# Kernel tuning notes

Hardware: AMD Instinct MI355X
Metric: run time of the kernel (lower is better)

## Reference

```python
import jax, jax.numpy as jnp
import numpy as np

B = 8192
DIMS = [1024, 1024, 1024, 1024]  # input, hidden0, hidden1, output
RANK = 64


def _apg_layer(x, Wm, bm, U, V, b, activate):
    # hyper-net (MLP_Layer with no hidden units == single Linear): generates rank*rank weights per sample
    w = (x @ Wm.T + bm).reshape(x.shape[0], RANK, RANK)   # [B, r, r]
    u = x @ U.T                                           # U_matrix: [B, r]
    # (u.unsqueeze(-1) * w).sum(-2) == per-sample matvec
    h = jnp.einsum('br,brs->bs', u, w)                    # [B, r]
    out = h @ V.T + b                                     # V_matrix + static bias: [B, out]
    return jax.nn.relu(out) if activate else out


def setup_inputs() -> dict:
    key = jax.random.key(0)
    ks = jax.random.split(key, 16)
    inp = {"x": jax.random.normal(ks[0], (B, DIMS[0]), dtype=jnp.float32)}
    ki = 1
    for l in range(3):
        din, dout = DIMS[l], DIMS[l + 1]
        inp[f"Wm{l}"] = jax.random.normal(ks[ki], (RANK * RANK, din), dtype=jnp.float32) * (1.0 / np.sqrt(din)); ki += 1
        inp[f"bm{l}"] = jnp.zeros((RANK * RANK,), dtype=jnp.float32)
        inp[f"U{l}"] = jax.random.normal(ks[ki], (RANK, din), dtype=jnp.float32) * (1.0 / np.sqrt(din)); ki += 1
        inp[f"V{l}"] = jax.random.normal(ks[ki], (dout, RANK), dtype=jnp.float32) * (1.0 / np.sqrt(RANK)); ki += 1
        inp[f"b{l}"] = jnp.zeros((dout,), dtype=jnp.float32)
    return inp


def reference(x, Wm0, bm0, U0, V0, b0, Wm1, bm1, U1, V1, b1, Wm2, bm2, U2, V2, b2):
    h = _apg_layer(x, Wm0, bm0, U0, V0, b0, activate=True)   # hidden layer 0 + ReLU
    h = _apg_layer(h, Wm1, bm1, U1, V1, b1, activate=True)   # hidden layer 1 + ReLU
    out = _apg_layer(h, Wm2, bm2, U2, V2, b2, activate=False)  # output layer, no activation
    return out
```

## Files before the change

kernel.cpp:

```cpp
#include <hip/hip_runtime.h>
#include <stdint.h>

typedef short bf16x8_t __attribute__((ext_vector_type(8)));
typedef short bf16x4_t __attribute__((ext_vector_type(4)));
typedef float f32x4_t __attribute__((ext_vector_type(4)));
typedef unsigned short u16x4_t __attribute__((ext_vector_type(4)));
typedef unsigned short u16x8_t __attribute__((ext_vector_type(8)));

#define DEV static __device__ __forceinline__

DEV float bf2f(unsigned short u) {
  union { unsigned int i; float f; } v; v.i = ((unsigned int)u) << 16; return v.f;
}
DEV unsigned short f2bf(float f) {
  union { float f; unsigned int i; } v; v.f = f;
  unsigned int x = v.i;
  unsigned int lsb = (x >> 16) & 1u;
  x += 0x7fffu + lsb;
  return (unsigned short)(x >> 16);
}

struct CvtSeg {
  const float* src[3];
  unsigned short* dst[3];
  int bstart[4];
};

DEV void cvt_block(const CvtSeg& cs, int vb, int tid) {
  int seg = (vb >= cs.bstart[1] ? 1 : 0) + (vb >= cs.bstart[2] ? 1 : 0);
  int local = (vb - cs.bstart[seg]) * 256 + tid;
  float4 v = ((const float4*)cs.src[seg])[local];
  u16x4_t o = { f2bf(v.x), f2bf(v.y), f2bf(v.z), f2bf(v.w) };
  *(u16x4_t*)&cs.dst[seg][local * 4] = o;
}

DEV void cvt_block512(const CvtSeg& cs, int vb, int tid) {
  int seg = (vb >= cs.bstart[1] ? 1 : 0) + (vb >= cs.bstart[2] ? 1 : 0);
  int local = (vb - cs.bstart[seg]) * 512 + tid;
  float4 v = ((const float4*)cs.src[seg])[local];
  u16x4_t o = { f2bf(v.x), f2bf(v.y), f2bf(v.z), f2bf(v.w) };
  *(u16x4_t*)&cs.dst[seg][local * 4] = o;
}

__global__ __launch_bounds__(256) void k_cvt(CvtSeg cs) {
  cvt_block(cs, blockIdx.x, threadIdx.x);
}

__global__ __launch_bounds__(256, 2) void xu_fused(
    const float* __restrict__ x,
    const unsigned short* __restrict__ U0,
    unsigned short* __restrict__ xb,
    unsigned short* __restrict__ u_out) {
  __shared__ unsigned short tlds[4 * 16 * 72];
  __shared__ float upart[4 * 16 * 68];

  const int tid = threadIdx.x;
  const int lane = tid & 63;
  const int w = tid >> 6;
  const int fr = lane & 15;
  const int quad = lane >> 4;
  const int rowBase = blockIdx.x * 16;

  unsigned short* tl = &tlds[w * 16 * 72];
  const int m2 = lane >> 2;
  const int kc = (lane & 3) * 16;

  f32x4_t uacc[4];
#pragma unroll
  for (int n = 0; n < 4; n++) uacc[n] = f32x4_t{0.f, 0.f, 0.f, 0.f};

  for (int it = 0; it < 4; ++it) {
    const int cb = w * 256 + it * 64;

    {
      const float* xp = x + (size_t)(rowBase + m2) * 1024 + cb + kc;
      float4 v0 = *(const float4*)(xp);
      float4 v1 = *(const float4*)(xp + 4);
      float4 v2 = *(const float4*)(xp + 8);
      float4 v3 = *(const float4*)(xp + 12);
      u16x8_t o0 = { f2bf(v0.x), f2bf(v0.y), f2bf(v0.z), f2bf(v0.w),
                     f2bf(v1.x), f2bf(v1.y), f2bf(v1.z), f2bf(v1.w) };
      u16x8_t o1 = { f2bf(v2.x), f2bf(v2.y), f2bf(v2.z), f2bf(v2.w),
                     f2bf(v3.x), f2bf(v3.y), f2bf(v3.z), f2bf(v3.w) };
      *(u16x8_t*)&tl[m2 * 72 + kc] = o0;
      *(u16x8_t*)&tl[m2 * 72 + kc + 8] = o1;
      unsigned short* xo = xb + (size_t)(rowBase + m2) * 1024 + cb + kc;
      *(u16x8_t*)xo = o0;
      *(u16x8_t*)(xo + 8) = o1;
    }

#pragma unroll
    for (int ks = 0; ks < 2; ++ks) {
      bf16x8_t at = *(const bf16x8_t*)&tl[fr * 72 + ks * 32 + quad * 8];
#pragma unroll
      for (int n = 0; n < 4; n++) {
        bf16x8_t bu = *(const bf16x8_t*)&U0[(size_t)(n * 16 + fr) * 1024 + cb +
                                            ks * 32 + quad * 8];
        uacc[n] = __builtin_amdgcn_mfma_f32_16x16x32_bf16(at, bu, uacc[n], 0, 0, 0);
      }
    }
  }

  {
    float* up = &upart[w * 16 * 68];
#pragma unroll
    for (int n = 0; n < 4; n++)
#pragma unroll
      for (int r = 0; r < 4; r++)
        up[(quad * 4 + r) * 68 + n * 16 + fr] = uacc[n][r];
  }
  __syncthreads();
  {
    int m = tid >> 4;
    int c0 = (tid & 15) * 4;
    f32x4_t s = {0.f, 0.f, 0.f, 0.f};
#pragma unroll
    for (int wv = 0; wv < 4; wv++)
      s += *(const f32x4_t*)&upart[wv * 16 * 68 + m * 68 + c0];
    u16x4_t o = { f2bf(s[0]), f2bf(s[1]), f2bf(s[2]), f2bf(s[3]) };
    *(u16x4_t*)&u_out[(size_t)(rowBase + m) * 64 + c0] = o;
  }
}

#define GLD(gp, lp)                                              \
  __builtin_amdgcn_global_load_lds(                              \
      (const __attribute__((address_space(1))) void*)(gp),       \
      (__attribute__((address_space(3))) void*)(lp), 16, 0, 0)

__global__ __launch_bounds__(512, 1) void k_hyper(
    const unsigned short* __restrict__ A,
    const unsigned short* __restrict__ Wmb,
    const unsigned short* __restrict__ ug,
    const float* __restrict__ bm,
    unsigned short* __restrict__ h_out,
    CvtSeg cs) {
  __shared__ unsigned short lds[65536];

  if (blockIdx.x >= 512) {
    cvt_block512(cs, blockIdx.x - 512, threadIdx.x);
    return;
  }

  unsigned short* As = lds;
  unsigned short* Bs = lds + 32768;

  const int tid = threadIdx.x;
  const int lane = tid & 63;
  const int w = tid >> 6;
  const int wr = w >> 2;
  const int wc = w & 3;
  const int bx = blockIdx.x & 15;
  const int by = blockIdx.x >> 4;
  const int rowBase = by * 256;
  const int colBase = bx * 256;
  const int fr = lane & 15;
  const int quad = lane >> 4;

  const int rl = lane >> 3;
  const int kbg = (lane & 7) ^ rl;
  const unsigned short* gA[4];
  const unsigned short* gB[4];
  int ldst[4];
#pragma unroll
  for (int h = 0; h < 2; h++)
#pragma unroll
    for (int jj = 0; jj < 2; jj++) {
      int tr = h * 128 + w * 16 + jj * 8 + rl;
      gA[h * 2 + jj] = A + (size_t)(rowBase + tr) * 1024 + kbg * 8;
      int ct = colBase + tr;
      gB[h * 2 + jj] =
          Wmb + (size_t)(((ct & 63) << 6) | (ct >> 6)) * 1024 + kbg * 8;
      ldst[h * 2 + jj] = (h * 128 + w * 16 + jj * 8) * 64;
    }

#define STAGE_ALL(t) do { const int db_ = ((t) & 1) * 16384;         \
    GLD(gA[0] + (t) * 64, &As[db_ + ldst[0]]);                       \
    GLD(gA[1] + (t) * 64, &As[db_ + ldst[1]]);                       \
    GLD(gA[2] + (t) * 64, &As[db_ + ldst[2]]);                       \
    GLD(gA[3] + (t) * 64, &As[db_ + ldst[3]]);                       \
    GLD(gB[0] + (t) * 64, &Bs[db_ + ldst[0]]);                       \
    GLD(gB[1] + (t) * 64, &Bs[db_ + ldst[1]]);                       \
    GLD(gB[2] + (t) * 64, &Bs[db_ + ldst[2]]);                       \
    GLD(gB[3] + (t) * 64, &Bs[db_ + ldst[3]]); } while (0)

  const int xors = fr & 7;
  const int aRow = (wr * 128 + fr) * 64;
  const int bRow = (wc * 64 + fr) * 64;
  const int slot0 = ((0 + quad) ^ xors) * 8;
  const int slot1 = ((4 + quad) ^ xors) * 8;

  f32x4_t acc[8][4];
#pragma unroll
  for (int i = 0; i < 8; i++)
#pragma unroll
    for (int j = 0; j < 4; j++) acc[i][j] = f32x4_t{0.f, 0.f, 0.f, 0.f};

  STAGE_ALL(0);
  asm volatile("s_waitcnt vmcnt(0)" ::: "memory");
  __builtin_amdgcn_s_barrier();

#pragma unroll 2
  for (int t = 0; t < 16; ++t) {
    const int d = (t & 1) * 16384;
    bf16x8_t a[8], b[4];
#pragma unroll
    for (int i = 0; i < 8; i++)
      a[i] = *(const bf16x8_t*)&As[d + aRow + i * 1024 + slot0];
#pragma unroll
    for (int j = 0; j < 4; j++)
      b[j] = *(const bf16x8_t*)&Bs[d + bRow + j * 1024 + slot0];
    if (t < 15) STAGE_ALL(t + 1);
    __builtin_amdgcn_s_barrier();
    asm volatile("s_waitcnt lgkmcnt(0)" ::: "memory");
    __builtin_amdgcn_sched_barrier(0);
    __builtin_amdgcn_s_setprio(1);
#pragma unroll
    for (int i = 0; i < 8; i++)
#pragma unroll
      for (int j = 0; j < 4; j++)
        acc[i][j] = __builtin_amdgcn_mfma_f32_16x16x32_bf16(a[i], b[j],
                                                            acc[i][j], 0, 0, 0);
    __builtin_amdgcn_s_setprio(0);
    __builtin_amdgcn_s_barrier();
#pragma unroll
    for (int i = 0; i < 8; i++)
      a[i] = *(const bf16x8_t*)&As[d + aRow + i * 1024 + slot1];
#pragma unroll
    for (int j = 0; j < 4; j++)
      b[j] = *(const bf16x8_t*)&Bs[d + bRow + j * 1024 + slot1];
    __builtin_amdgcn_s_barrier();
    asm volatile("s_waitcnt lgkmcnt(0)" ::: "memory");
    __builtin_amdgcn_sched_barrier(0);
    __builtin_amdgcn_s_setprio(1);
#pragma unroll
    for (int i = 0; i < 8; i++)
#pragma unroll
      for (int j = 0; j < 4; j++)
        acc[i][j] = __builtin_amdgcn_mfma_f32_16x16x32_bf16(a[i], b[j],
                                                            acc[i][j], 0, 0, 0);
    __builtin_amdgcn_s_setprio(0);
    asm volatile("s_waitcnt vmcnt(0)" ::: "memory");
    __builtin_amdgcn_s_barrier();
  }

  __syncthreads();

  {
    int row = tid >> 1;
    int c0 = (tid & 1) * 32;
    const unsigned short* up = ug + (size_t)(rowBase + row) * 64 + c0;
    bf16x8_t v0 = *(const bf16x8_t*)(up);
    bf16x8_t v1 = *(const bf16x8_t*)(up + 8);
    bf16x8_t v2 = *(const bf16x8_t*)(up + 16);
    bf16x8_t v3 = *(const bf16x8_t*)(up + 24);
#pragma unroll
    for (int m = 0; m < 8; m++) {
      lds[(c0 + m) * 264 + row] = (unsigned short)v0[m];
      lds[(c0 + 8 + m) * 264 + row] = (unsigned short)v1[m];
      lds[(c0 + 16 + m) * 264 + row] = (unsigned short)v2[m];
      lds[(c0 + 24 + m) * 264 + row] = (unsigned short)v3[m];
    }
  }
  __syncthreads();

  const int s = bx * 4 + wc;
  float bmv[4];
#pragma unroll
  for (int j = 0; j < 4; j++) bmv[j] = bm[(j * 16 + fr) * 64 + s];

#pragma unroll
  for (int i = 0; i < 8; i++) {
    int row0 = wr * 128 + i * 16 + quad * 4;
    bf16x4_t uv[4];
#pragma unroll
    for (int j = 0; j < 4; j++)
      uv[j] = *(const bf16x4_t*)&lds[(j * 16 + fr) * 264 + row0];
#pragma unroll
    for (int r = 0; r < 4; r++) {
      float p = 0.f;
#pragma unroll
      for (int j = 0; j < 4; j++)
        p += bf2f((unsigned short)uv[j][r]) * (acc[i][j][r] + bmv[j]);
      p += __shfl_xor(p, 1, 64);
      p += __shfl_xor(p, 2, 64);
      p += __shfl_xor(p, 4, 64);
      p += __shfl_xor(p, 8, 64);
      if (fr == 0)
        h_out[(size_t)(rowBase + row0 + r) * 64 + s] = f2bf(p);
    }
  }
}

__global__ __launch_bounds__(256, 2) void vu_fused(
    const unsigned short* __restrict__ h,
    const unsigned short* __restrict__ Vb,
    const float* __restrict__ bias,
    const unsigned short* __restrict__ Un,
    unsigned short* __restrict__ act,
    unsigned short* __restrict__ u_out) {
  __shared__ unsigned short tlds[4 * 16 * 72];
  __shared__ float upart[4 * 16 * 68];

  const int tid = threadIdx.x;
  const int lane = tid & 63;
  const int w = tid >> 6;
  const int fr = lane & 15;
  const int quad = lane >> 4;
  const int rowBase = blockIdx.x * 16;

  unsigned short* tl = &tlds[w * 16 * 72];

  bf16x8_t ah0 = *(const bf16x8_t*)&h[(size_t)(rowBase + fr) * 64 + quad * 8];
  bf16x8_t ah1 = *(const bf16x8_t*)&h[(size_t)(rowBase + fr) * 64 + 32 + quad * 8];

  f32x4_t uacc[4];
#pragma unroll
  for (int n = 0; n < 4; n++) uacc[n] = f32x4_t{0.f, 0.f, 0.f, 0.f};

  for (int it = 0; it < 4; ++it) {
    const int cb = w * 256 + it * 64;

    f32x4_t tacc[4];
#pragma unroll
    for (int nt = 0; nt < 4; nt++) {
      const unsigned short* vrow = Vb + (size_t)(cb + nt * 16 + fr) * 64;
      bf16x8_t b0 = *(const bf16x8_t*)&vrow[quad * 8];
      bf16x8_t b1 = *(const bf16x8_t*)&vrow[32 + quad * 8];
      f32x4_t z = {0.f, 0.f, 0.f, 0.f};
      z = __builtin_amdgcn_mfma_f32_16x16x32_bf16(ah0, b0, z, 0, 0, 0);
      tacc[nt] = __builtin_amdgcn_mfma_f32_16x16x32_bf16(ah1, b1, z, 0, 0, 0);
    }

#pragma unroll
    for (int nt = 0; nt < 4; nt++) {
      float bv = bias[cb + nt * 16 + fr];
#pragma unroll
      for (int r = 0; r < 4; r++) {
        float v = tacc[nt][r] + bv;
        v = v > 0.f ? v : 0.f;
        tl[(quad * 4 + r) * 72 + nt * 16 + fr] = f2bf(v);
      }
    }

    {
      int m2 = lane >> 2;
      int kc = (lane & 3) * 16;
      bf16x8_t t0 = *(const bf16x8_t*)&tl[m2 * 72 + kc];
      bf16x8_t t1 = *(const bf16x8_t*)&tl[m2 * 72 + kc + 8];
      unsigned short* ap = act + (size_t)(rowBase + m2) * 1024 + cb + kc;
      *(bf16x8_t*)ap = t0;
      *(bf16x8_t*)(ap + 8) = t1;
    }

#pragma unroll
    for (int ks = 0; ks < 2; ++ks) {
      bf16x8_t at = *(const bf16x8_t*)&tl[fr * 72 + ks * 32 + quad * 8];
#pragma unroll
      for (int n = 0; n < 4; n++) {
        bf16x8_t bu = *(const bf16x8_t*)&Un[(size_t)(n * 16 + fr) * 1024 + cb +
                                            ks * 32 + quad * 8];
        uacc[n] = __builtin_amdgcn_mfma_f32_16x16x32_bf16(at, bu, uacc[n], 0, 0, 0);
      }
    }
  }

  {
    float* up = &upart[w * 16 * 68];
#pragma unroll
    for (int n = 0; n < 4; n++)
#pragma unroll
      for (int r = 0; r < 4; r++)
        up[(quad * 4 + r) * 68 + n * 16 + fr] = uacc[n][r];
  }
  __syncthreads();
  {
    int m = tid >> 4;
    int c0 = (tid & 15) * 4;
    f32x4_t s = {0.f, 0.f, 0.f, 0.f};
#pragma unroll
    for (int wv = 0; wv < 4; wv++)
      s += *(const f32x4_t*)&upart[wv * 16 * 68 + m * 68 + c0];
    u16x4_t o = { f2bf(s[0]), f2bf(s[1]), f2bf(s[2]), f2bf(s[3]) };
    *(u16x4_t*)&u_out[(size_t)(rowBase + m) * 64 + c0] = o;
  }
}

__global__ __launch_bounds__(256, 2) void k_final(
    const unsigned short* __restrict__ A, const unsigned short* __restrict__ B,
    const float* __restrict__ bias, float* __restrict__ Cout) {
  __shared__ unsigned short As[128 * 64];
  __shared__ unsigned short Bs[128 * 64];

  const int tid = threadIdx.x;
  const int lane = tid & 63;
  const int w = tid >> 6;
  const int wrow0 = (w & 1) * 64;
  const int wcol0 = (w >> 1) * 64;
  const int rowBase = blockIdx.y * 128;
  const int colBase = blockIdx.x * 128;

  const int rl = lane >> 3;
  const int kbg = (lane & 7) ^ rl;
  const int fr = lane & 15;
  const int quad = lane >> 4;

  f32x4_t acc[4][4];
#pragma unroll
  for (int i = 0; i < 4; i++)
#pragma unroll
    for (int j = 0; j < 4; j++) acc[i][j] = f32x4_t{0.f, 0.f, 0.f, 0.f};

  __syncthreads();
#pragma unroll
  for (int jj = 0; jj < 4; ++jj) {
    int tr = w * 32 + jj * 8 + rl;
    const unsigned short* ga = A + (size_t)(rowBase + tr) * 64 + kbg * 8;
    const unsigned short* gb = B + (size_t)(colBase + tr) * 64 + kbg * 8;
    __builtin_amdgcn_global_load_lds(
        (const __attribute__((address_space(1))) void*)ga,
        (__attribute__((address_space(3))) void*)&As[(w * 32 + jj * 8) * 64],
        16, 0, 0);
    __builtin_amdgcn_global_load_lds(
        (const __attribute__((address_space(1))) void*)gb,
        (__attribute__((address_space(3))) void*)&Bs[(w * 32 + jj * 8) * 64],
        16, 0, 0);
  }
  __syncthreads();

#pragma unroll
  for (int ks = 0; ks < 2; ++ks) {
    bf16x8_t a[4], b[4];
#pragma unroll
    for (int i = 0; i < 4; i++) {
      int m = wrow0 + i * 16 + fr;
      int slot = (ks * 4 + quad) ^ (m & 7);
      a[i] = *(const bf16x8_t*)&As[m * 64 + slot * 8];
    }
#pragma unroll
    for (int j = 0; j < 4; j++) {
      int n = wcol0 + j * 16 + fr;
      int slot = (ks * 4 + quad) ^ (n & 7);
      b[j] = *(const bf16x8_t*)&Bs[n * 64 + slot * 8];
    }
#pragma unroll
    for (int i = 0; i < 4; i++)
#pragma unroll
      for (int j = 0; j < 4; j++)
        acc[i][j] = __builtin_amdgcn_mfma_f32_16x16x32_bf16(a[i], b[j],
                                                            acc[i][j], 0, 0, 0);
  }

#pragma unroll
  for (int j = 0; j < 4; j++) {
    int col = colBase + wcol0 + j * 16 + fr;
    float bv = bias[col];
#pragma unroll
    for (int i = 0; i < 4; i++) {
#pragma unroll
      for (int r = 0; r < 4; r++) {
        int row = rowBase + wrow0 + i * 16 + quad * 4 + r;
        Cout[(size_t)row * 1024 + col] = acc[i][j][r] + bv;
      }
    }
  }
}

extern "C" void kernel_launch(void* const* d_in, const int* in_sizes, int n_in,
                              void* d_out, int out_size, void* d_ws,
                              size_t ws_size, hipStream_t stream) {
  const float* x = (const float*)d_in[0];
  const float* Wm[3] = {(const float*)d_in[1], (const float*)d_in[6], (const float*)d_in[11]};
  const float* bm[3] = {(const float*)d_in[2], (const float*)d_in[7], (const float*)d_in[12]};
  const float* U[3]  = {(const float*)d_in[3], (const float*)d_in[8], (const float*)d_in[13]};
  const float* V[3]  = {(const float*)d_in[4], (const float*)d_in[9], (const float*)d_in[14]};
  const float* bs[3] = {(const float*)d_in[5], (const float*)d_in[10], (const float*)d_in[15]};

  char* p = (char*)d_ws;
  unsigned short* xb = (unsigned short*)p;  p += 8192UL * 1024 * 2;
  unsigned short* act = (unsigned short*)p; p += 8192UL * 1024 * 2;
  unsigned short* Wmb[3];
  for (int l = 0; l < 3; l++) { Wmb[l] = (unsigned short*)p; p += 4096UL * 1024 * 2; }
  unsigned short* Ub[3];
  for (int l = 0; l < 3; l++) { Ub[l] = (unsigned short*)p; p += 64UL * 1024 * 2; }
  unsigned short* Vb[3];
  for (int l = 0; l < 3; l++) { Vb[l] = (unsigned short*)p; p += 1024UL * 64 * 2; }
  unsigned short* hb = (unsigned short*)p;  p += 8192UL * 64 * 2;
  unsigned short* ug = (unsigned short*)p;  p += 8192UL * 64 * 2;

  CvtSeg c0;
  c0.src[0] = Wm[0]; c0.dst[0] = Wmb[0];
  c0.src[1] = U[0];  c0.dst[1] = Ub[0];
  c0.src[2] = U[0];  c0.dst[2] = Ub[0];
  c0.bstart[0] = 0; c0.bstart[1] = 4096; c0.bstart[2] = 4160; c0.bstart[3] = 4160;
  k_cvt<<<4160, 256, 0, stream>>>(c0);

  xu_fused<<<512, 256, 0, stream>>>(x, Ub[0], xb, ug);

  CvtSeg ch[3];
  ch[0].src[0] = Wm[1]; ch[0].dst[0] = Wmb[1];
  ch[0].src[1] = U[1];  ch[0].dst[1] = Ub[1];
  ch[0].src[2] = V[0];  ch[0].dst[2] = Vb[0];
  ch[0].bstart[0] = 0; ch[0].bstart[1] = 2048; ch[0].bstart[2] = 2080; ch[0].bstart[3] = 2112;
  ch[1].src[0] = Wm[2]; ch[1].dst[0] = Wmb[2];
  ch[1].src[1] = U[2];  ch[1].dst[1] = Ub[2];
  ch[1].src[2] = V[1];  ch[1].dst[2] = Vb[1];
  ch[1].bstart[0] = 0; ch[1].bstart[1] = 2048; ch[1].bstart[2] = 2080; ch[1].bstart[3] = 2112;
  ch[2].src[0] = V[2]; ch[2].dst[0] = Vb[2];
  ch[2].src[1] = V[2]; ch[2].dst[1] = Vb[2];
  ch[2].src[2] = V[2]; ch[2].dst[2] = Vb[2];
  ch[2].bstart[0] = 0; ch[2].bstart[1] = 32; ch[2].bstart[2] = 32; ch[2].bstart[3] = 32;

  const int hyperGrid[3] = {512 + 2112, 512 + 2112, 512 + 32};

  const unsigned short* cur = xb;
  for (int l = 0; l < 3; l++) {
    k_hyper<<<hyperGrid[l], 512, 0, stream>>>(cur, Wmb[l], ug, bm[l], hb, ch[l]);
    if (l < 2) {
      vu_fused<<<512, 256, 0, stream>>>(hb, Vb[l], bs[l], Ub[l + 1], act, ug);
      cur = act;
    } else {
      k_final<<<dim3(8, 64), 256, 0, stream>>>(hb, Vb[2], bs[2], (float*)d_out);
    }
  }
}
```

Baseline: 426.7 us.

## Split main GEMM staging into quarter-tile phases and coalesce final-layer stores via LDS

The main hyper-weight GEMM loop now loads A and B tiles in four half-panels and stages the next tile's pieces one at a time between four MFMA phases. Partial vmcnt waits replace full drains, so global-to-LDS copies overlap the matrix math more finely. The final output kernel now stages its accumulators through an LDS panel and writes full rows with float4 stores instead of scattered scalar stores. This adds more barriers and a more complex waitcnt schedule, which could hurt if the counts are mis-tuned.

```diff
diff --git a/kernel.cpp b/kernel.cpp
--- a/kernel.cpp
+++ b/kernel.cpp
@@ -156,38 +156,52 @@
   const int fr = lane & 15;
   const int quad = lane >> 4;
 
-  const int rl = lane >> 3;
-  const int kbg = (lane & 7) ^ rl;
-  const unsigned short* gA[4];
-  const unsigned short* gB[4];
-  int ldst[4];
-#pragma unroll
-  for (int h = 0; h < 2; h++)
-#pragma unroll
-    for (int jj = 0; jj < 2; jj++) {
-      int tr = h * 128 + w * 16 + jj * 8 + rl;
-      gA[h * 2 + jj] = A + (size_t)(rowBase + tr) * 1024 + kbg * 8;
-      int ct = colBase + tr;
-      gB[h * 2 + jj] =
-          Wmb + (size_t)(((ct & 63) << 6) | (ct >> 6)) * 1024 + kbg * 8;
-      ldst[h * 2 + jj] = (h * 128 + w * 16 + jj * 8) * 64;
-    }
-
-#define STAGE_ALL(t) do { const int db_ = ((t) & 1) * 16384;         \
-    GLD(gA[0] + (t) * 64, &As[db_ + ldst[0]]);                       \
-    GLD(gA[1] + (t) * 64, &As[db_ + ldst[1]]);                       \
-    GLD(gA[2] + (t) * 64, &As[db_ + ldst[2]]);                       \
-    GLD(gA[3] + (t) * 64, &As[db_ + ldst[3]]);                       \
-    GLD(gB[0] + (t) * 64, &Bs[db_ + ldst[0]]);                       \
-    GLD(gB[1] + (t) * 64, &Bs[db_ + ldst[1]]);                       \
-    GLD(gB[2] + (t) * 64, &Bs[db_ + ldst[2]]);                       \
-    GLD(gB[3] + (t) * 64, &Bs[db_ + ldst[3]]); } while (0)
-
-  const int xors = fr & 7;
-  const int aRow = (wr * 128 + fr) * 64;
-  const int bRow = (wc * 64 + fr) * 64;
-  const int slot0 = ((0 + quad) ^ xors) * 8;
-  const int slot1 = ((4 + quad) ^ xors) * 8;
+  const int rl8 = lane >> 3;
+  const int kbg = (lane & 7) ^ rl8;
+  const int wb = w * 8 + rl8;
+
+  const unsigned short* gAbase =
+      A + (size_t)(rowBase + wb) * 1024 + kbg * 8;
+
+  const int wb5 = wb >> 5;
+  const int wb31 = wb & 31;
+  int ctl00 = (0 * 2 + wb5) * 64 + 0 * 32 + wb31;
+  int ctl01 = (1 * 2 + wb5) * 64 + 0 * 32 + wb31;
+  int ctl10 = (0 * 2 + wb5) * 64 + 1 * 32 + wb31;
+  int ctl11 = (1 * 2 + wb5) * 64 + 1 * 32 + wb31;
+  int ct;
+  ct = colBase + ctl00;
+  const unsigned short* gB00 =
+      Wmb + (size_t)(((ct & 63) << 6) | (ct >> 6)) * 1024 + kbg * 8;
+  ct = colBase + ctl01;
+  const unsigned short* gB01 =
+      Wmb + (size_t)(((ct & 63) << 6) | (ct >> 6)) * 1024 + kbg * 8;
+  ct = colBase + ctl10;
+  const unsigned short* gB10 =
+      Wmb + (size_t)(((ct & 63) << 6) | (ct >> 6)) * 1024 + kbg * 8;
+  ct = colBase + ctl11;
+  const unsigned short* gB11 =
+      Wmb + (size_t)(((ct & 63) << 6) | (ct >> 6)) * 1024 + kbg * 8;
+
+  const int ldw = (w * 8) * 64;
+
+#define STAGE_A0(tt) do { const int l_ = (((tt)&1)*16384) + 0*8192 + ldw;   \
+    GLD(gAbase + (size_t)0 * 1024 + (tt) * 64, &As[l_]);                    \
+    GLD(gAbase + (size_t)128 * 1024 + (tt) * 64, &As[l_ + 4096]); } while (0)
+#define STAGE_A1(tt) do { const int l_ = (((tt)&1)*16384) + 1*8192 + ldw;   \
+    GLD(gAbase + (size_t)64 * 1024 + (tt) * 64, &As[l_]);                   \
+    GLD(gAbase + (size_t)192 * 1024 + (tt) * 64, &As[l_ + 4096]); } while (0)
+#define STAGE_B0(tt) do { const int l_ = (((tt)&1)*16384) + 0*8192 + ldw;   \
+    GLD(gB00 + (tt) * 64, &Bs[l_]);                                         \
+    GLD(gB01 + (tt) * 64, &Bs[l_ + 4096]); } while (0)
+#define STAGE_B1(tt) do { const int l_ = (((tt)&1)*16384) + 1*8192 + ldw;   \
+    GLD(gB10 + (tt) * 64, &Bs[l_]);                                         \
+    GLD(gB11 + (tt) * 64, &Bs[l_ + 4096]); } while (0)
+
+  const int slot0 = ((0 + quad) ^ (fr & 7)) * 8;
+  const int slot1 = ((4 + quad) ^ (fr & 7)) * 8;
+  const int aRow = (wr * 64 + fr) * 64;
+  const int bRow = (wc * 32 + fr) * 64;
 
   f32x4_t acc[8][4];
 #pragma unroll
@@ -195,51 +209,107 @@
 #pragma unroll
     for (int j = 0; j < 4; j++) acc[i][j] = f32x4_t{0.f, 0.f, 0.f, 0.f};
 
-  STAGE_ALL(0);
-  asm volatile("s_waitcnt vmcnt(0)" ::: "memory");
+  STAGE_A0(0); STAGE_B0(0); STAGE_B1(0); STAGE_A1(0);
+  asm volatile("s_waitcnt vmcnt(4)" ::: "memory");
   __builtin_amdgcn_s_barrier();
 
 #pragma unroll 2
   for (int t = 0; t < 16; ++t) {
     const int d = (t & 1) * 16384;
-    bf16x8_t a[8], b[4];
-#pragma unroll
-    for (int i = 0; i < 8; i++)
-      a[i] = *(const bf16x8_t*)&As[d + aRow + i * 1024 + slot0];
-#pragma unroll
-    for (int j = 0; j < 4; j++)
-      b[j] = *(const bf16x8_t*)&Bs[d + bRow + j * 1024 + slot0];
-    if (t < 15) STAGE_ALL(t + 1);
+    bf16x8_t am[4][2], bn[2][2], bn1[2][2];
+#pragma unroll
+    for (int i = 0; i < 4; i++) {
+      am[i][0] = *(const bf16x8_t*)&As[d + aRow + i * 1024 + slot0];
+      am[i][1] = *(const bf16x8_t*)&As[d + aRow + i * 1024 + slot1];
+    }
+#pragma unroll
+    for (int j = 0; j < 2; j++) {
+      bn[j][0] = *(const bf16x8_t*)&Bs[d + bRow + j * 1024 + slot0];
+      bn[j][1] = *(const bf16x8_t*)&Bs[d + bRow + j * 1024 + slot1];
+    }
+    if (t < 15) STAGE_A0(t + 1);
     __builtin_amdgcn_s_barrier();
     asm volatile("s_waitcnt lgkmcnt(0)" ::: "memory");
     __builtin_amdgcn_sched_barrier(0);
     __builtin_amdgcn_s_setprio(1);
 #pragma unroll
-    for (int i = 0; i < 8; i++)
-#pragma unroll
-      for (int j = 0; j < 4; j++)
-        acc[i][j] = __builtin_amdgcn_mfma_f32_16x16x32_bf16(a[i], b[j],
+    for (int i = 0; i < 4; i++)
+#pragma unroll
+      for (int j = 0; j < 2; j++) {
+        acc[i][j] = __builtin_amdgcn_mfma_f32_16x16x32_bf16(am[i][0], bn[j][0],
                                                             acc[i][j], 0, 0, 0);
+        acc[i][j] = __builtin_amdgcn_mfma_f32_16x16x32_bf16(am[i][1], bn[j][1],
+                                                            acc[i][j], 0, 0, 0);
+      }
     __builtin_amdgcn_s_setprio(0);
-    __builtin_amdgcn_s_barrier();
-#pragma unroll
-    for (int i = 0; i < 8; i++)
-      a[i] = *(const bf16x8_t*)&As[d + aRow + i * 1024 + slot1];
-#pragma unroll
-    for (int j = 0; j < 4; j++)
-      b[j] = *(const bf16x8_t*)&Bs[d + bRow + j * 1024 + slot1];
+    if (t < 15) { asm volatile("s_waitcnt vmcnt(4)" ::: "memory"); }
+    else        { asm volatile("s_waitcnt vmcnt(2)" ::: "memory"); }
+    __builtin_amdgcn_s_barrier();
+#pragma unroll
+    for (int j = 0; j < 2; j++) {
+      bn1[j][0] = *(const bf16x8_t*)&Bs[d + 8192 + bRow + j * 1024 + slot0];
+      bn1[j][1] = *(const bf16x8_t*)&Bs[d + 8192 + bRow + j * 1024 + slot1];
+    }
+    if (t < 15) STAGE_B0(t + 1);
     __builtin_amdgcn_s_barrier();
     asm volatile("s_waitcnt lgkmcnt(0)" ::: "memory");
     __builtin_amdgcn_sched_barrier(0);
     __builtin_amdgcn_s_setprio(1);
 #pragma unroll
-    for (int i = 0; i < 8; i++)
-#pragma unroll
-      for (int j = 0; j < 4; j++)
-        acc[i][j] = __builtin_amdgcn_mfma_f32_16x16x32_bf16(a[i], b[j],
-                                                            acc[i][j], 0, 0, 0);
+    for (int i = 0; i < 4; i++)
+#pragma unroll
+      for (int j = 0; j < 2; j++) {
+        acc[i][2 + j] = __builtin_amdgcn_mfma_f32_16x16x32_bf16(
+            am[i][0], bn1[j][0], acc[i][2 + j], 0, 0, 0);
+        acc[i][2 + j] = __builtin_amdgcn_mfma_f32_16x16x32_bf16(
+            am[i][1], bn1[j][1], acc[i][2 + j], 0, 0, 0);
+      }
     __builtin_amdgcn_s_setprio(0);
-    asm volatile("s_waitcnt vmcnt(0)" ::: "memory");
+    if (t < 15) { asm volatile("s_waitcnt vmcnt(4)" ::: "memory"); }
+    else        { asm volatile("s_waitcnt vmcnt(0)" ::: "memory"); }
+    __builtin_amdgcn_s_barrier();
+#pragma unroll
+    for (int i = 0; i < 4; i++) {
+      am[i][0] = *(const bf16x8_t*)&As[d + 8192 + aRow + i * 1024 + slot0];
+      am[i][1] = *(const bf16x8_t*)&As[d + 8192 + aRow + i * 1024 + slot1];
+    }
+    if (t < 15) STAGE_B1(t + 1);
+    __builtin_amdgcn_s_barrier();
+    asm volatile("s_waitcnt lgkmcnt(0)" ::: "memory");
+    __builtin_amdgcn_sched_barrier(0);
+    __builtin_amdgcn_s_setprio(1);
+#pragma unroll
+    for (int i = 0; i < 4; i++)
+#pragma unroll
+      for (int j = 0; j < 2; j++) {
+        acc[4 + i][2 + j] = __builtin_amdgcn_mfma_f32_16x16x32_bf16(
+            am[i][0], bn1[j][0], acc[4 + i][2 + j], 0, 0, 0);
+        acc[4 + i][2 + j] = __builtin_amdgcn_mfma_f32_16x16x32_bf16(
+            am[i][1], bn1[j][1], acc[4 + i][2 + j], 0, 0, 0);
+      }
+    __builtin_amdgcn_s_setprio(0);
+    __builtin_amdgcn_s_barrier();
+#pragma unroll
+    for (int j = 0; j < 2; j++) {
+      bn[j][0] = *(const bf16x8_t*)&Bs[d + bRow + j * 1024 + slot0];
+      bn[j][1] = *(const bf16x8_t*)&Bs[d + bRow + j * 1024 + slot1];
+    }
+    if (t < 15) STAGE_A1(t + 1);
+    __builtin_amdgcn_s_barrier();
+    asm volatile("s_waitcnt lgkmcnt(0)" ::: "memory");
+    __builtin_amdgcn_sched_barrier(0);
+    __builtin_amdgcn_s_setprio(1);
+#pragma unroll
+    for (int i = 0; i < 4; i++)
+#pragma unroll
+      for (int j = 0; j < 2; j++) {
+        acc[4 + i][j] = __builtin_amdgcn_mfma_f32_16x16x32_bf16(
+            am[i][0], bn[j][0], acc[4 + i][j], 0, 0, 0);
+        acc[4 + i][j] = __builtin_amdgcn_mfma_f32_16x16x32_bf16(
+            am[i][1], bn[j][1], acc[4 + i][j], 0, 0, 0);
+      }
+    __builtin_amdgcn_s_setprio(0);
+    if (t < 15) { asm volatile("s_waitcnt vmcnt(4)" ::: "memory"); }
     __builtin_amdgcn_s_barrier();
   }
 
@@ -388,8 +458,12 @@
 __global__ __launch_bounds__(256, 2) void k_final(
     const unsigned short* __restrict__ A, const unsigned short* __restrict__ B,
     const float* __restrict__ bias, float* __restrict__ Cout) {
-  __shared__ unsigned short As[128 * 64];
-  __shared__ unsigned short Bs[128 * 64];
+  __shared__ union {
+    unsigned short ab[2][128 * 64];
+    float pan[2][128 * 33];
+  } sm;
+  unsigned short* As = sm.ab[0];
+  unsigned short* Bs = sm.ab[1];
 
   const int tid = threadIdx.x;
   const int lane = tid & 63;
@@ -410,7 +484,6 @@
 #pragma unroll
     for (int j = 0; j < 4; j++) acc[i][j] = f32x4_t{0.f, 0.f, 0.f, 0.f};
 
-  __syncthreads();
 #pragma unroll
   for (int jj = 0; jj < 4; ++jj) {
     int tr = w * 32 + jj * 8 + rl;
@@ -450,16 +523,45 @@
                                                             acc[i][j], 0, 0, 0);
   }
 
-#pragma unroll
-  for (int j = 0; j < 4; j++) {
-    int col = colBase + wcol0 + j * 16 + fr;
-    float bv = bias[col];
-#pragma unroll
-    for (int i = 0; i < 4; i++) {
-#pragma unroll
-      for (int r = 0; r < 4; r++) {
-        int row = rowBase + wrow0 + i * 16 + quad * 4 + r;
-        Cout[(size_t)row * 1024 + col] = acc[i][j][r] + bv;
+  float bv[4];
+#pragma unroll
+  for (int j = 0; j < 4; j++) bv[j] = bias[colBase + wcol0 + j * 16 + fr];
+
+#pragma unroll
+  for (int rp = 0; rp < 2; ++rp) {
+    __syncthreads();
+    {
+      float* P = sm.pan[w >> 1];
+#pragma unroll
+      for (int jj = 0; jj < 2; ++jj) {
+        int j = rp * 2 + jj;
+        int colp = jj * 16 + fr;
+#pragma unroll
+        for (int i = 0; i < 4; i++)
+#pragma unroll
+          for (int r = 0; r < 4; r++) {
+            int row = wrow0 + i * 16 + quad * 4 + r;
+            P[row * 33 + colp] = acc[i][j][r] + bv[j];
+          }
+      }
+    }
+    __syncthreads();
+    {
+      int row = tid >> 1;
+      int ch = (tid & 1) * 16;
+#pragma unroll
+      for (int pb = 0; pb < 2; ++pb) {
+        const float* Pr = &sm.pan[pb][row * 33 + ch];
+        float4 v0 = { Pr[0],  Pr[1],  Pr[2],  Pr[3]  };
+        float4 v1 = { Pr[4],  Pr[5],  Pr[6],  Pr[7]  };
+        float4 v2 = { Pr[8],  Pr[9],  Pr[10], Pr[11] };
+        float4 v3 = { Pr[12], Pr[13], Pr[14], Pr[15] };
+        float* out = &Cout[(size_t)(rowBase + row) * 1024 + colBase + pb * 64 +
+                           rp * 32 + ch];
+        ((float4*)out)[0] = v0;
+        ((float4*)out)[1] = v1;
+        ((float4*)out)[2] = v2;
+        ((float4*)out)[3] = v3;
       }
     }
   }
```

Measured after the change: 417.8 us. -2.1%, faster.
